# Optimization experiments

Hardware: AMD Instinct MI355X
Metric: run time of the kernel (lower is better)

Reference implementation:

```python
import jax, jax.numpy as jnp
import numpy as np

B, T, D, H = 256, 128, 256, 512
L = 2  # label_size


def _lstm_scan(xs, Wih, Whh, b):
    """xs: [T,B,Din]; Wih: [4H,Din]; Whh: [4H,H]; b: [4H]. Returns h_seq [T,B,H], (hT,cT).
    PyTorch LSTMCell gate order: i, f, g, o."""
    Hh = Whh.shape[1]

    def step(carry, xt):
        h, c = carry
        gates = xt @ Wih.T + h @ Whh.T + b  # [B,4H]
        i, f, g, o = jnp.split(gates, 4, axis=-1)
        c = jax.nn.sigmoid(f) * c + jax.nn.sigmoid(i) * jnp.tanh(g)
        h = jax.nn.sigmoid(o) * jnp.tanh(c)
        return (h, c), h

    Bt = xs.shape[1]
    h0 = jnp.zeros((Bt, Hh), xs.dtype)
    c0 = jnp.zeros((Bt, Hh), xs.dtype)
    (hT, cT), hs = jax.lax.scan(step, (h0, c0), xs)
    return hs, (hT, cT)


def setup_inputs() -> dict:
    key = jax.random.key(0)
    ks = jax.random.split(key, 8)

    def xavier(k, shape):
        fan_in, fan_out = shape[1], shape[0]
        std = np.sqrt(2.0 / (fan_in + fan_out))
        return jax.random.normal(k, shape, jnp.float32) * std

    return {
        "x": jax.random.normal(ks[0], (B, T, D), jnp.float32),
        "Wf_ih": xavier(ks[1], (4 * H, D)),
        "Wf_hh": xavier(ks[2], (4 * H, H)),
        "bf": jnp.zeros((4 * H,), jnp.float32),
        "Wb_ih": xavier(ks[3], (4 * H, D)),
        "Wb_hh": xavier(ks[4], (4 * H, H)),
        "bb": jnp.zeros((4 * H,), jnp.float32),
        "Ws_ih": xavier(ks[5], (8 * H, 2 * H)),
        "Ws_hh": xavier(ks[6], (8 * H, 2 * H)),
        "bs": jnp.zeros((8 * H,), jnp.float32),
        "Wl": xavier(ks[7], (L, 2 * H)),
        "bl": jnp.zeros((L,), jnp.float32),
    }


def reference(x, Wf_ih, Wf_hh, bf, Wb_ih, Wb_hh, bb, Ws_ih, Ws_hh, bs, Wl, bl):
    # Dropout is identity in eval mode (deterministic reference).
    xs = jnp.swapaxes(x, 0, 1)  # [T,B,D]
    f_seq, _ = _lstm_scan(xs, Wf_ih, Wf_hh, bf)          # forward over t=0..T-1
    b_seq, _ = _lstm_scan(xs[::-1], Wb_ih, Wb_hh, bb)    # backward over t=T-1..0, in append order
    # Faithful to source: zip(f, b) pairs f[i] with b[i] (b in reverse-time append order).
    combined = jnp.concatenate([f_seq, b_seq], axis=-1)  # [T,B,2H]
    _, (hs, _) = _lstm_scan(combined, Ws_ih, Ws_hh, bs)  # final hidden [B,2H]
    return jax.nn.sigmoid(hs @ Wl.T + bl)                # [B,L]
```

## Files before the change

kernel.cpp:

```cpp
#include <hip/hip_runtime.h>
#include <math.h>

#define BB 256
#define TT 128
#define DD 256
#define HH 512

typedef __bf16 bf16x8 __attribute__((ext_vector_type(8)));
typedef float  f32x4  __attribute__((ext_vector_type(4)));

__device__ inline unsigned short f2bf(float f) {
  unsigned u = __builtin_bit_cast(unsigned, f);
  unsigned r = (u + 0x7fffu + ((u >> 16) & 1u)) >> 16;
  return (unsigned short)r;
}
__device__ inline float bf2f(unsigned short h) {
  unsigned u = ((unsigned)h) << 16;
  return __builtin_bit_cast(float, u);
}
__device__ inline float sigm(float x)   { return 1.f / (1.f + __expf(-x)); }
__device__ inline float tanh_f(float x) { return 2.f / (1.f + __expf(-2.f * x)) - 1.f; }

__device__ __forceinline__ void gl16(const void* g, void* l) {
  __builtin_amdgcn_global_load_lds(
      (const __attribute__((address_space(1))) unsigned int*)g,
      (__attribute__((address_space(3))) unsigned int*)l, 16, 0, 0);
}

__device__ __forceinline__ void vmw8() { asm volatile("s_waitcnt vmcnt(8)" ::: "memory"); }
__device__ __forceinline__ void vmw4() { asm volatile("s_waitcnt vmcnt(4)" ::: "memory"); }
__device__ __forceinline__ void vmw0() { asm volatile("s_waitcnt vmcnt(0)" ::: "memory"); }

__global__ void prep(const float* __restrict__ x,
                     const float* __restrict__ Wf_ih, const float* __restrict__ Wf_hh, const float* __restrict__ bf_,
                     const float* __restrict__ Wb_ih, const float* __restrict__ Wb_hh, const float* __restrict__ bb_,
                     const float* __restrict__ Ws_ih, const float* __restrict__ Ws_hh, const float* __restrict__ bs_,
                     unsigned short* __restrict__ xb, unsigned short* __restrict__ Wpf,
                     unsigned short* __restrict__ Wpb, unsigned short* __restrict__ Wps,
                     float* __restrict__ bpf, float* __restrict__ bpb, float* __restrict__ bps,
                     unsigned short* __restrict__ comb, unsigned short* __restrict__ hs,
                     float* __restrict__ cf, float* __restrict__ cb, float* __restrict__ cs) {
  const long gid = (long)blockIdx.x * blockDim.x + threadIdx.x;
  const long stride = (long)gridDim.x * blockDim.x;

  for (long i = gid; i < (long)BB * TT * DD; i += stride) {
    long k = i % DD;
    long bt = i / DD;
    long t = bt % TT;
    long b = bt / TT;
    xb[(t * BB + b) * DD + k] = f2bf(x[i]);
  }
  for (long i = gid; i < 2048L * 768; i += stride) {
    int n = (int)(i / 768), k = (int)(i - (long)n * 768);
    int j = n >> 2, g = n & 3;
    float vf = (k < DD) ? Wf_ih[(size_t)(g * HH + j) * DD + k]
                        : Wf_hh[(size_t)(g * HH + j) * HH + (k - DD)];
    float vb = (k < DD) ? Wb_ih[(size_t)(g * HH + j) * DD + k]
                        : Wb_hh[(size_t)(g * HH + j) * HH + (k - DD)];
    Wpf[i] = f2bf(vf);
    Wpb[i] = f2bf(vb);
  }
  for (long i = gid; i < 4096L * 2048; i += stride) {
    int n = (int)(i >> 11), k = (int)(i & 2047);
    int j = n >> 2, g = n & 3;
    float v = (k < 1024) ? Ws_ih[(size_t)(g * 1024 + j) * 1024 + k]
                         : Ws_hh[(size_t)(g * 1024 + j) * 1024 + (k - 1024)];
    Wps[i] = f2bf(v);
  }
  for (long i = gid; i < 2048; i += stride) {
    int j = (int)(i >> 2), g = (int)(i & 3);
    bpf[i] = bf_[g * HH + j];
    bpb[i] = bb_[g * HH + j];
  }
  for (long i = gid; i < 4096; i += stride) {
    int j = (int)(i >> 2), g = (int)(i & 3);
    bps[i] = bs_[g * 1024 + j];
  }
  for (long i = gid; i < (long)BB * 1024; i += stride) comb[i] = 0;
  for (long i = gid; i < 2L * BB * 1024; i += stride) hs[i] = 0;
  for (long i = gid; i < (long)BB * HH; i += stride) { cf[i] = 0.f; cb[i] = 0.f; }
  for (long i = gid; i < (long)BB * 1024; i += stride) cs[i] = 0.f;
}

template<int NKS, int KSPLIT>
__device__ __forceinline__ void gemm_tile_lds(
    const unsigned short* __restrict__ a0, long as0,
    const unsigned short* __restrict__ a1, long as1,
    const unsigned short* __restrict__ wb, long ws,
    char* sm, int tid, f32x4 (&acc)[4]) {
  const int rl   = tid >> 3;
  const int eb   = (tid & 7) * 16;
  const int kel  = (eb ^ ((rl & 7) << 4)) >> 1;
  const int wuni = (tid >> 6) * 1024;

  const int lane = tid & 63;
  const int w    = tid >> 6;
  const int ln   = lane & 15;
  const int q    = lane >> 4;
  const int swzr = (ln & 7) << 4;
  const int col  = w * 16 + ln;

  auto stage = [&](int buf, int k0) {
    char* lA = sm + buf * 16384;
    char* lB = lA + 8192;
    const unsigned short* ab = (k0 < KSPLIT) ? (a0 + k0) : (a1 + (k0 - KSPLIT));
    const long astr = (k0 < KSPLIT) ? as0 : as1;
#pragma unroll
    for (int h = 0; h < 2; ++h) {
      const int row = h * 32 + rl;
      gl16(ab + (long)row * astr + kel, lA + h * 4096 + wuni);
      gl16(wb + (long)row * ws + k0 + kel, lB + h * 4096 + wuni);
    }
  };

  stage(0, 0); stage(1, 64); stage(2, 128);

#pragma unroll 3
  for (int ks = 0; ks < NKS; ++ks) {
    if (ks < NKS - 2)       vmw8();
    else if (ks == NKS - 2) vmw4();
    else                    vmw0();
    __builtin_amdgcn_sched_barrier(0);
    __builtin_amdgcn_s_barrier();
    __builtin_amdgcn_sched_barrier(0);
    const char* lA = sm + (ks % 3) * 16384;
    const char* lB = lA + 8192;
#pragma unroll
    for (int ks2 = 0; ks2 < 2; ++ks2) {
      const int eo = (ks2 * 64 + q * 16) ^ swzr;
      const bf16x8 bf = *reinterpret_cast<const bf16x8*>(lB + col * 128 + eo);
#pragma unroll
      for (int mb = 0; mb < 4; ++mb) {
        const bf16x8 af = *reinterpret_cast<const bf16x8*>(lA + (mb * 16 + ln) * 128 + eo);
        acc[mb] = __builtin_amdgcn_mfma_f32_16x16x32_bf16(af, bf, acc[mb], 0, 0, 0);
      }
    }
    __builtin_amdgcn_sched_barrier(0);
    __builtin_amdgcn_s_barrier();
    __builtin_amdgcn_sched_barrier(0);
    if (ks + 3 < NKS) stage(ks % 3, (ks + 3) * 64);
  }
}

__global__ __launch_bounds__(256, 2) void phase(int p,
    const unsigned short* __restrict__ xb,
    const unsigned short* __restrict__ Wpf, const unsigned short* __restrict__ Wpb,
    const float* __restrict__ bpf, const float* __restrict__ bpb,
    unsigned short* __restrict__ comb, float* __restrict__ cf, float* __restrict__ cb,
    const unsigned short* __restrict__ Wps, const float* __restrict__ bps,
    unsigned short* __restrict__ hs, float* __restrict__ cs) {
  __shared__ __align__(16) char sm[49152];
  const int bi = blockIdx.x;
  const int tid = threadIdx.x;
  const int w = tid >> 6;
  const int lane = tid & 63;
  const int q = lane >> 4;
  const int ln = lane & 15;
  const int col = w * 16 + ln;
  float* scratch = (float*)sm;

  if (bi < 256) {
    const int t = p;
    if (t >= TT) return;
    const int xcd = bi & 7;
    const int idx = bi >> 3;
    const int m0 = (idx & 3) * 64;
    const int slot = idx >> 2;
    const int panel = xcd * 8 + slot;
    const int dir = panel & 1;
    const int n0 = (panel >> 1) * 64;
    const unsigned short* __restrict__ W = dir ? Wpb : Wpf;
    const float* __restrict__ bias = dir ? bpb : bpf;
    float* __restrict__ cbuf = dir ? cb : cf;
    const int dofs = dir ? HH : 0;
    const int tx = dir ? (TT - 1 - t) : t;

    f32x4 acc[4];
#pragma unroll
    for (int mb = 0; mb < 4; ++mb) acc[mb] = (f32x4){0.f, 0.f, 0.f, 0.f};
    gemm_tile_lds<768 / 64, DD>(
        xb + ((long)tx * BB + m0) * DD, DD,
        comb + ((long)t * BB + m0) * 1024 + dofs, 1024,
        W + (long)n0 * 768, 768, sm, tid, acc);

#pragma unroll
    for (int mb = 0; mb < 4; ++mb)
#pragma unroll
      for (int r = 0; r < 4; ++r)
        scratch[(mb * 16 + q * 4 + r) * 68 + col] = acc[mb][r];
    __syncthreads();

#pragma unroll
    for (int r = 0; r < 4; ++r) {
      const int cid = tid + r * 256;
      const int bl = cid >> 4;
      const int jl = cid & 15;
      const int b = m0 + bl;
      const int j = (n0 >> 2) + jl;
      const f32x4 g  = *reinterpret_cast<const f32x4*>(&scratch[bl * 68 + jl * 4]);
      const f32x4 bv = *reinterpret_cast<const f32x4*>(&bias[n0 + jl * 4]);
      const float gi = g[0] + bv[0];
      const float gf = g[1] + bv[1];
      const float gg = g[2] + bv[2];
      const float go = g[3] + bv[3];
      const float c_old = cbuf[(size_t)b * HH + j];
      const float c_new = sigm(gf) * c_old + sigm(gi) * tanh_f(gg);
      const float h = sigm(go) * tanh_f(c_new);
      cbuf[(size_t)b * HH + j] = c_new;
      comb[((size_t)(t + 1) * BB + b) * 1024 + dofs + j] = f2bf(h);
    }
  } else {
    if (p < 1) return;
    const int s = p - 1;
    const int bb2 = bi - 256;
    const int xcd = bb2 & 7;
    const int idx = bb2 >> 3;
    const int m0 = (idx & 3) * 64;
    const int n0 = (xcd * 8 + (idx >> 2)) * 64;

    f32x4 acc[4];
#pragma unroll
    for (int mb = 0; mb < 4; ++mb) acc[mb] = (f32x4){0.f, 0.f, 0.f, 0.f};
    gemm_tile_lds<2048 / 64, 1024>(
        comb + ((long)p * BB + m0) * 1024, 1024,
        hs + ((long)(s & 1) * BB + m0) * 1024, 1024,
        Wps + (long)n0 * 2048, 2048, sm, tid, acc);

#pragma unroll
    for (int mb = 0; mb < 4; ++mb)
#pragma unroll
      for (int r = 0; r < 4; ++r)
        scratch[(mb * 16 + q * 4 + r) * 68 + col] = acc[mb][r];
    __syncthreads();

#pragma unroll
    for (int r = 0; r < 4; ++r) {
      const int cid = tid + r * 256;
      const int bl = cid >> 4;
      const int jl = cid & 15;
      const int b = m0 + bl;
      const int j = (n0 >> 2) + jl;
      const f32x4 g  = *reinterpret_cast<const f32x4*>(&scratch[bl * 68 + jl * 4]);
      const f32x4 bv = *reinterpret_cast<const f32x4*>(&bps[n0 + jl * 4]);
      const float gi = g[0] + bv[0];
      const float gf = g[1] + bv[1];
      const float gg = g[2] + bv[2];
      const float go = g[3] + bv[3];
      const float c_old = cs[(size_t)b * 1024 + j];
      const float c_new = sigm(gf) * c_old + sigm(gi) * tanh_f(gg);
      const float h = sigm(go) * tanh_f(c_new);
      cs[(size_t)b * 1024 + j] = c_new;
      hs[((size_t)((s + 1) & 1) * BB + b) * 1024 + j] = f2bf(h);
    }
  }
}

__global__ __launch_bounds__(256) void classifier(const unsigned short* __restrict__ hs,
                                                  const float* __restrict__ Wl,
                                                  const float* __restrict__ bl,
                                                  float* __restrict__ out) {
  const int b = blockIdx.x;
  const int tid = threadIdx.x;
  const unsigned short* hb = hs + (size_t)b * 1024;
  float s0 = 0.f, s1 = 0.f;
#pragma unroll
  for (int kk = 0; kk < 4; ++kk) {
    const int k = tid * 4 + kk;
    const float hv = bf2f(hb[k]);
    s0 += hv * Wl[k];
    s1 += hv * Wl[1024 + k];
  }
  for (int off = 32; off > 0; off >>= 1) {
    s0 += __shfl_down(s0, off);
    s1 += __shfl_down(s1, off);
  }
  __shared__ float red[8];
  const int w = tid >> 6;
  if ((tid & 63) == 0) { red[w * 2] = s0; red[w * 2 + 1] = s1; }
  __syncthreads();
  if (tid == 0) {
    const float l0 = red[0] + red[2] + red[4] + red[6] + bl[0];
    const float l1 = red[1] + red[3] + red[5] + red[7] + bl[1];
    out[b * 2 + 0] = sigm(l0);
    out[b * 2 + 1] = sigm(l1);
  }
}

extern "C" void kernel_launch(void* const* d_in, const int* in_sizes, int n_in,
                              void* d_out, int out_size, void* d_ws, size_t ws_size,
                              hipStream_t stream) {
  const float* x     = (const float*)d_in[0];
  const float* Wf_ih = (const float*)d_in[1];
  const float* Wf_hh = (const float*)d_in[2];
  const float* bf_   = (const float*)d_in[3];
  const float* Wb_ih = (const float*)d_in[4];
  const float* Wb_hh = (const float*)d_in[5];
  const float* bb_   = (const float*)d_in[6];
  const float* Ws_ih = (const float*)d_in[7];
  const float* Ws_hh = (const float*)d_in[8];
  const float* bs_   = (const float*)d_in[9];
  const float* Wl    = (const float*)d_in[10];
  const float* bl    = (const float*)d_in[11];
  float* out = (float*)d_out;

  char* ws = (char*)d_ws;
  size_t off = 0;
  auto take = [&](size_t bytes) -> void* {
    void* p = ws + off;
    off += (bytes + 255) & ~(size_t)255;
    return p;
  };
  unsigned short* xb   = (unsigned short*)take((size_t)BB * TT * DD * 2);
  unsigned short* Wpf  = (unsigned short*)take((size_t)2048 * 768 * 2);
  unsigned short* Wpb  = (unsigned short*)take((size_t)2048 * 768 * 2);
  unsigned short* Wps  = (unsigned short*)take((size_t)4096 * 2048 * 2);
  float* bpf = (float*)take(2048 * 4);
  float* bpb = (float*)take(2048 * 4);
  float* bps = (float*)take(4096 * 4);
  unsigned short* comb = (unsigned short*)take((size_t)(TT + 1) * BB * 1024 * 2);
  unsigned short* hs   = (unsigned short*)take((size_t)2 * BB * 1024 * 2);
  float* cf = (float*)take((size_t)BB * HH * 4);
  float* cb = (float*)take((size_t)BB * HH * 4);
  float* cs = (float*)take((size_t)BB * 1024 * 4);

  prep<<<2048, 256, 0, stream>>>(x, Wf_ih, Wf_hh, bf_, Wb_ih, Wb_hh, bb_,
                                 Ws_ih, Ws_hh, bs_, xb, Wpf, Wpb, Wps,
                                 bpf, bpb, bps, comb, hs, cf, cb, cs);
  for (int p = 0; p <= TT; ++p)
    phase<<<512, 256, 0, stream>>>(p, xb, Wpf, Wpb, bpf, bpb, comb, cf, cb,
                                   Wps, bps, hs, cs);
  classifier<<<256, 256, 0, stream>>>(hs, Wl, bl, out);
}
```

Before: 1.751 ms.

## Split stacked LSTM gate GEMM into pipelined input and recurrent halves

The second-layer LSTM's input projection (over the combined bi-LSTM output) is split from its recurrent projection. The input half now runs one phase earlier in its own group of blocks and writes fp32 gate pre-activations to a double-buffered global buffer. The recurrent half then only does a K=1024 GEMM on the critical path and adds the precomputed gates. The grid grows to 768 blocks and the launch count by one. In exchange it adds an extra fp32 gate buffer write and read each step and raises the occupancy hint to 3 blocks per CU.

```diff
diff --git a/kernel.cpp b/kernel.cpp
--- a/kernel.cpp
+++ b/kernel.cpp
@@ -142,13 +142,13 @@
   }
 }
 
-__global__ __launch_bounds__(256, 2) void phase(int p,
+__global__ __launch_bounds__(256, 3) void phase(int p,
     const unsigned short* __restrict__ xb,
     const unsigned short* __restrict__ Wpf, const unsigned short* __restrict__ Wpb,
     const float* __restrict__ bpf, const float* __restrict__ bpb,
     unsigned short* __restrict__ comb, float* __restrict__ cf, float* __restrict__ cb,
     const unsigned short* __restrict__ Wps, const float* __restrict__ bps,
-    unsigned short* __restrict__ hs, float* __restrict__ cs) {
+    float* __restrict__ Gs, unsigned short* __restrict__ hs, float* __restrict__ cs) {
   __shared__ __align__(16) char sm[49152];
   const int bi = blockIdx.x;
   const int tid = threadIdx.x;
@@ -209,9 +209,8 @@
       cbuf[(size_t)b * HH + j] = c_new;
       comb[((size_t)(t + 1) * BB + b) * 1024 + dofs + j] = f2bf(h);
     }
-  } else {
-    if (p < 1) return;
-    const int s = p - 1;
+  } else if (bi < 512) {
+    if (p < 1 || p > TT) return;
     const int bb2 = bi - 256;
     const int xcd = bb2 & 7;
     const int idx = bb2 >> 3;
@@ -221,10 +220,33 @@
     f32x4 acc[4];
 #pragma unroll
     for (int mb = 0; mb < 4; ++mb) acc[mb] = (f32x4){0.f, 0.f, 0.f, 0.f};
-    gemm_tile_lds<2048 / 64, 1024>(
-        comb + ((long)p * BB + m0) * 1024, 1024,
-        hs + ((long)(s & 1) * BB + m0) * 1024, 1024,
-        Wps + (long)n0 * 2048, 2048, sm, tid, acc);
+    const unsigned short* ca = comb + ((long)p * BB + m0) * 1024;
+    gemm_tile_lds<1024 / 64, 2048>(ca, 1024, ca, 1024,
+                                   Wps + (long)n0 * 2048, 2048, sm, tid, acc);
+
+    float* __restrict__ G = Gs + (size_t)((p - 1) & 1) * BB * 4096;
+#pragma unroll
+    for (int mb = 0; mb < 4; ++mb)
+#pragma unroll
+      for (int r = 0; r < 4; ++r) {
+        const int row = m0 + mb * 16 + q * 4 + r;
+        G[(size_t)row * 4096 + n0 + col] = acc[mb][r];
+      }
+  } else {
+    if (p < 2 || p > TT + 1) return;
+    const int s = p - 2;
+    const int bb2 = bi - 512;
+    const int xcd = bb2 & 7;
+    const int idx = bb2 >> 3;
+    const int m0 = (idx & 3) * 64;
+    const int n0 = (xcd * 8 + (idx >> 2)) * 64;
+
+    f32x4 acc[4];
+#pragma unroll
+    for (int mb = 0; mb < 4; ++mb) acc[mb] = (f32x4){0.f, 0.f, 0.f, 0.f};
+    const unsigned short* ha = hs + ((long)(s & 1) * BB + m0) * 1024;
+    gemm_tile_lds<1024 / 64, 2048>(ha, 1024, ha, 1024,
+                                   Wps + (long)n0 * 2048 + 1024, 2048, sm, tid, acc);
 
 #pragma unroll
     for (int mb = 0; mb < 4; ++mb)
@@ -233,6 +255,7 @@
         scratch[(mb * 16 + q * 4 + r) * 68 + col] = acc[mb][r];
     __syncthreads();
 
+    const float* __restrict__ G = Gs + (size_t)(s & 1) * BB * 4096;
 #pragma unroll
     for (int r = 0; r < 4; ++r) {
       const int cid = tid + r * 256;
@@ -240,12 +263,13 @@
       const int jl = cid & 15;
       const int b = m0 + bl;
       const int j = (n0 >> 2) + jl;
-      const f32x4 g  = *reinterpret_cast<const f32x4*>(&scratch[bl * 68 + jl * 4]);
-      const f32x4 bv = *reinterpret_cast<const f32x4*>(&bps[n0 + jl * 4]);
-      const float gi = g[0] + bv[0];
-      const float gf = g[1] + bv[1];
-      const float gg = g[2] + bv[2];
-      const float go = g[3] + bv[3];
+      const f32x4 g   = *reinterpret_cast<const f32x4*>(&scratch[bl * 68 + jl * 4]);
+      const f32x4 gin = *reinterpret_cast<const f32x4*>(&G[(size_t)b * 4096 + n0 + jl * 4]);
+      const f32x4 bv  = *reinterpret_cast<const f32x4*>(&bps[n0 + jl * 4]);
+      const float gi = g[0] + gin[0] + bv[0];
+      const float gf = g[1] + gin[1] + bv[1];
+      const float gg = g[2] + gin[2] + bv[2];
+      const float go = g[3] + gin[3] + bv[3];
       const float c_old = cs[(size_t)b * 1024 + j];
       const float c_new = sigm(gf) * c_old + sigm(gi) * tanh_f(gg);
       const float h = sigm(go) * tanh_f(c_new);
@@ -322,12 +346,13 @@
   float* cf = (float*)take((size_t)BB * HH * 4);
   float* cb = (float*)take((size_t)BB * HH * 4);
   float* cs = (float*)take((size_t)BB * 1024 * 4);
+  float* Gs = (float*)take((size_t)2 * BB * 4096 * 4);
 
   prep<<<2048, 256, 0, stream>>>(x, Wf_ih, Wf_hh, bf_, Wb_ih, Wb_hh, bb_,
                                  Ws_ih, Ws_hh, bs_, xb, Wpf, Wpb, Wps,
                                  bpf, bpb, bps, comb, hs, cf, cb, cs);
-  for (int p = 0; p <= TT; ++p)
-    phase<<<512, 256, 0, stream>>>(p, xb, Wpf, Wpb, bpf, bpb, comb, cf, cb,
-                                   Wps, bps, hs, cs);
+  for (int p = 0; p < TT + 2; ++p)
+    phase<<<768, 256, 0, stream>>>(p, xb, Wpf, Wpb, bpf, bpb, comb, cf, cb,
+                                   Wps, bps, Gs, hs, cs);
   classifier<<<256, 256, 0, stream>>>(hs, Wl, bl, out);
 }
```

New measurement: 1.763 ms. About the same (+0.7%).

## Split K across waves with full 64x64 per-wave tiles and LDS reduction

Applied to the files above, without the earlier changes.

Each wave now computes the whole 64x64 output tile over its own quarter of the K steps, instead of a 64x16 column slice over all of K. It keeps a 4x4 grid of accumulators, and the four partial sums are added in an enlarged LDS scratch region before the gate math. The aim is to reuse each A fragment across four B fragments and cut LDS fragment reads per MFMA. The cost is that the K loop and its barriers are unchanged, so only one wave issues MFMAs at each step while the other three wait. The change also raises register pressure and LDS size per block.

```diff
diff --git a/kernel.cpp b/kernel.cpp
--- a/kernel.cpp
+++ b/kernel.cpp
@@ -87,7 +87,8 @@
     const unsigned short* __restrict__ a0, long as0,
     const unsigned short* __restrict__ a1, long as1,
     const unsigned short* __restrict__ wb, long ws,
-    char* sm, int tid, f32x4 (&acc)[4]) {
+    char* sm, int tid, f32x4 (&acc)[4][4]) {
+  constexpr int QS = NKS / 4;
   const int rl   = tid >> 3;
   const int eb   = (tid & 7) * 16;
   const int kel  = (eb ^ ((rl & 7) << 4)) >> 1;
@@ -98,7 +99,6 @@
   const int ln   = lane & 15;
   const int q    = lane >> 4;
   const int swzr = (ln & 7) << 4;
-  const int col  = w * 16 + ln;
 
   auto stage = [&](int buf, int k0) {
     char* lA = sm + buf * 16384;
@@ -123,16 +123,24 @@
     __builtin_amdgcn_sched_barrier(0);
     __builtin_amdgcn_s_barrier();
     __builtin_amdgcn_sched_barrier(0);
-    const char* lA = sm + (ks % 3) * 16384;
-    const char* lB = lA + 8192;
-#pragma unroll
-    for (int ks2 = 0; ks2 < 2; ++ks2) {
-      const int eo = (ks2 * 64 + q * 16) ^ swzr;
-      const bf16x8 bf = *reinterpret_cast<const bf16x8*>(lB + col * 128 + eo);
-#pragma unroll
-      for (int mb = 0; mb < 4; ++mb) {
-        const bf16x8 af = *reinterpret_cast<const bf16x8*>(lA + (mb * 16 + ln) * 128 + eo);
-        acc[mb] = __builtin_amdgcn_mfma_f32_16x16x32_bf16(af, bf, acc[mb], 0, 0, 0);
+    if (ks / QS == w) {
+      const char* lA = sm + (ks % 3) * 16384;
+      const char* lB = lA + 8192;
+#pragma unroll
+      for (int ks2 = 0; ks2 < 2; ++ks2) {
+        const int eo = (ks2 * 64 + q * 16) ^ swzr;
+        bf16x8 af[4], bf[4];
+#pragma unroll
+        for (int mb = 0; mb < 4; ++mb)
+          af[mb] = *reinterpret_cast<const bf16x8*>(lA + (mb * 16 + ln) * 128 + eo);
+#pragma unroll
+        for (int nf = 0; nf < 4; ++nf)
+          bf[nf] = *reinterpret_cast<const bf16x8*>(lB + (nf * 16 + ln) * 128 + eo);
+#pragma unroll
+        for (int mb = 0; mb < 4; ++mb)
+#pragma unroll
+          for (int nf = 0; nf < 4; ++nf)
+            acc[mb][nf] = __builtin_amdgcn_mfma_f32_16x16x32_bf16(af[mb], bf[nf], acc[mb][nf], 0, 0, 0);
       }
     }
     __builtin_amdgcn_sched_barrier(0);
@@ -141,6 +149,8 @@
     if (ks + 3 < NKS) stage(ks % 3, (ks + 3) * 64);
   }
 }
+
+#define RGN 4352
 
 __global__ __launch_bounds__(256, 2) void phase(int p,
     const unsigned short* __restrict__ xb,
@@ -149,14 +159,13 @@
     unsigned short* __restrict__ comb, float* __restrict__ cf, float* __restrict__ cb,
     const unsigned short* __restrict__ Wps, const float* __restrict__ bps,
     unsigned short* __restrict__ hs, float* __restrict__ cs) {
-  __shared__ __align__(16) char sm[49152];
+  __shared__ __align__(16) char sm[4 * RGN * 4];
   const int bi = blockIdx.x;
   const int tid = threadIdx.x;
   const int w = tid >> 6;
   const int lane = tid & 63;
   const int q = lane >> 4;
   const int ln = lane & 15;
-  const int col = w * 16 + ln;
   float* scratch = (float*)sm;
 
   if (bi < 256) {
@@ -175,9 +184,11 @@
     const int dofs = dir ? HH : 0;
     const int tx = dir ? (TT - 1 - t) : t;
 
-    f32x4 acc[4];
-#pragma unroll
-    for (int mb = 0; mb < 4; ++mb) acc[mb] = (f32x4){0.f, 0.f, 0.f, 0.f};
+    f32x4 acc[4][4];
+#pragma unroll
+    for (int mb = 0; mb < 4; ++mb)
+#pragma unroll
+      for (int nf = 0; nf < 4; ++nf) acc[mb][nf] = (f32x4){0.f, 0.f, 0.f, 0.f};
     gemm_tile_lds<768 / 64, DD>(
         xb + ((long)tx * BB + m0) * DD, DD,
         comb + ((long)t * BB + m0) * 1024 + dofs, 1024,
@@ -186,8 +197,10 @@
 #pragma unroll
     for (int mb = 0; mb < 4; ++mb)
 #pragma unroll
-      for (int r = 0; r < 4; ++r)
-        scratch[(mb * 16 + q * 4 + r) * 68 + col] = acc[mb][r];
+      for (int nf = 0; nf < 4; ++nf)
+#pragma unroll
+        for (int r = 0; r < 4; ++r)
+          scratch[w * RGN + (mb * 16 + q * 4 + r) * 68 + nf * 16 + ln] = acc[mb][nf][r];
     __syncthreads();
 
 #pragma unroll
@@ -197,12 +210,16 @@
       const int jl = cid & 15;
       const int b = m0 + bl;
       const int j = (n0 >> 2) + jl;
-      const f32x4 g  = *reinterpret_cast<const f32x4*>(&scratch[bl * 68 + jl * 4]);
+      const int o = bl * 68 + jl * 4;
+      const f32x4 g0 = *reinterpret_cast<const f32x4*>(&scratch[o]);
+      const f32x4 g1 = *reinterpret_cast<const f32x4*>(&scratch[RGN + o]);
+      const f32x4 g2 = *reinterpret_cast<const f32x4*>(&scratch[2 * RGN + o]);
+      const f32x4 g3 = *reinterpret_cast<const f32x4*>(&scratch[3 * RGN + o]);
       const f32x4 bv = *reinterpret_cast<const f32x4*>(&bias[n0 + jl * 4]);
-      const float gi = g[0] + bv[0];
-      const float gf = g[1] + bv[1];
-      const float gg = g[2] + bv[2];
-      const float go = g[3] + bv[3];
+      const float gi = g0[0] + g1[0] + g2[0] + g3[0] + bv[0];
+      const float gf = g0[1] + g1[1] + g2[1] + g3[1] + bv[1];
+      const float gg = g0[2] + g1[2] + g2[2] + g3[2] + bv[2];
+      const float go = g0[3] + g1[3] + g2[3] + g3[3] + bv[3];
       const float c_old = cbuf[(size_t)b * HH + j];
       const float c_new = sigm(gf) * c_old + sigm(gi) * tanh_f(gg);
       const float h = sigm(go) * tanh_f(c_new);
@@ -218,9 +235,11 @@
     const int m0 = (idx & 3) * 64;
     const int n0 = (xcd * 8 + (idx >> 2)) * 64;
 
-    f32x4 acc[4];
-#pragma unroll
-    for (int mb = 0; mb < 4; ++mb) acc[mb] = (f32x4){0.f, 0.f, 0.f, 0.f};
+    f32x4 acc[4][4];
+#pragma unroll
+    for (int mb = 0; mb < 4; ++mb)
+#pragma unroll
+      for (int nf = 0; nf < 4; ++nf) acc[mb][nf] = (f32x4){0.f, 0.f, 0.f, 0.f};
     gemm_tile_lds<2048 / 64, 1024>(
         comb + ((long)p * BB + m0) * 1024, 1024,
         hs + ((long)(s & 1) * BB + m0) * 1024, 1024,
@@ -229,8 +248,10 @@
 #pragma unroll
     for (int mb = 0; mb < 4; ++mb)
 #pragma unroll
-      for (int r = 0; r < 4; ++r)
-        scratch[(mb * 16 + q * 4 + r) * 68 + col] = acc[mb][r];
+      for (int nf = 0; nf < 4; ++nf)
+#pragma unroll
+        for (int r = 0; r < 4; ++r)
+          scratch[w * RGN + (mb * 16 + q * 4 + r) * 68 + nf * 16 + ln] = acc[mb][nf][r];
     __syncthreads();
 
 #pragma unroll
@@ -240,12 +261,16 @@
       const int jl = cid & 15;
       const int b = m0 + bl;
       const int j = (n0 >> 2) + jl;
-      const f32x4 g  = *reinterpret_cast<const f32x4*>(&scratch[bl * 68 + jl * 4]);
+      const int o = bl * 68 + jl * 4;
+      const f32x4 g0 = *reinterpret_cast<const f32x4*>(&scratch[o]);
+      const f32x4 g1 = *reinterpret_cast<const f32x4*>(&scratch[RGN + o]);
+      const f32x4 g2 = *reinterpret_cast<const f32x4*>(&scratch[2 * RGN + o]);
+      const f32x4 g3 = *reinterpret_cast<const f32x4*>(&scratch[3 * RGN + o]);
       const f32x4 bv = *reinterpret_cast<const f32x4*>(&bps[n0 + jl * 4]);
-      const float gi = g[0] + bv[0];
-      const float gf = g[1] + bv[1];
-      const float gg = g[2] + bv[2];
-      const float go = g[3] + bv[3];
+      const float gi = g0[0] + g1[0] + g2[0] + g3[0] + bv[0];
+      const float gf = g0[1] + g1[1] + g2[1] + g3[1] + bv[1];
+      const float gg = g0[2] + g1[2] + g2[2] + g3[2] + bv[2];
+      const float go = g0[3] + g1[3] + g2[3] + g3[3] + bv[3];
       const float c_old = cs[(size_t)b * 1024 + j];
       const float c_new = sigm(gf) * c_old + sigm(gi) * tanh_f(gg);
       const float h = sigm(go) * tanh_f(c_new);
```

Result: slower. 2.598 ms (+48.4%).
